# Optimization experiments

Hardware: AMD Instinct MI355X
Metric: run time of the kernel (lower is better)

## Reference

```python
import jax, jax.numpy as jnp
import numpy as np

N_NODES = 1_000_000
N_EDGES = 32_000_000
DC = 16
HIDDEN = 32
EPS = 1e-8
LN_EPS = 1e-5


def _harmonic_encoding(x, dC):
    # x: [n] curvature in [-1,1]; returns [n, dC] (dC even here)
    norm = jnp.clip((x + 1.0) / (2.0 + EPS), 0.0, 1.0)
    freqs = jnp.arange(1, dC // 2 + 1, dtype=x.dtype) * jnp.pi  # [dC/2]
    ang = norm[:, None] * freqs[None, :]                        # [n, dC/2]
    # interleave sin/cos exactly like torch.stack(...,dim=2).view(n,dC)
    return jnp.stack([jnp.sin(ang), jnp.cos(ang)], axis=2).reshape(x.shape[0], dC)


def setup_inputs() -> dict:
    key = jax.random.key(0)
    k_orc, k_ei, k_w1, k_w2, k_g = jax.random.split(key, 5)
    node_orc = jax.random.uniform(k_orc, (N_NODES,), dtype=jnp.float32) * 2.0 - 1.0
    edge_index = jax.random.randint(k_ei, (2, N_EDGES), 0, N_NODES, dtype=jnp.int64)
    # MLP params (torch Linear convention: W [out, in])
    W1 = jax.random.normal(k_w1, (HIDDEN, DC), dtype=jnp.float32) * (1.0 / np.sqrt(DC))
    b1 = jnp.zeros((HIDDEN,), dtype=jnp.float32)
    W2 = jax.random.normal(k_w2, (DC, HIDDEN), dtype=jnp.float32) * (1.0 / np.sqrt(HIDDEN))
    b2 = jnp.zeros((DC,), dtype=jnp.float32)
    gamma = jnp.ones((DC,), dtype=jnp.float32)
    beta = jnp.zeros((DC,), dtype=jnp.float32)
    return {"node_orc": node_orc, "edge_index": edge_index,
            "W1": W1, "b1": b1, "W2": W2, "b2": b2,
            "gamma": gamma, "beta": beta}


def _neighbor_mean(node_orc, edge_index):
    src, dst = edge_index[0], edge_index[1]
    n = node_orc.shape[0]
    deg = jnp.zeros((n,), node_orc.dtype).at[src].add(1.0).at[dst].add(1.0)
    s = (jnp.zeros((n,), node_orc.dtype)
         .at[src].add(node_orc[dst])
         .at[dst].add(node_orc[src]))
    return jnp.where(deg > 0, s / jnp.where(deg > 0, deg, 1.0), 0.0)


def reference(node_orc, edge_index, W1, b1, W2, b2, gamma, beta):
    # advanced harmonic encoding: node encoding + neighbor-mean encoding
    nb_mean = _neighbor_mean(node_orc, edge_index)
    Phi_base = jnp.concatenate(
        [_harmonic_encoding(node_orc, DC // 2),
         _harmonic_encoding(nb_mean, DC // 2)], axis=1)      # [n, 16]
    # learnable MLP (dropout in eval = identity) + LayerNorm + residual
    h = jax.nn.relu(jnp.einsum('nd,hd->nh', Phi_base, W1) + b1)
    y = jnp.einsum('nh,dh->nd', h, W2) + b2
    mu = jnp.mean(y, axis=-1, keepdims=True)
    var = jnp.var(y, axis=-1, keepdims=True)
    y = (y - mu) / jnp.sqrt(var + LN_EPS) * gamma + beta
    return y + Phi_base
```

## Files before the change

kernel.cpp:

```cpp
#include <hip/hip_runtime.h>
#include <hip/hip_bf16.h>

constexpr int kNodes = 1000000;
constexpr int kEdges = 32000000;

constexpr int NB = 256;
constexpr int BSHIFT = 12;
constexpr int BNODES = 4096;
constexpr int NBUSED = (kNodes + BNODES - 1) / BNODES;
constexpr int EPT = 4096;
constexpr int TILES = (kEdges + EPT - 1) / EPT;
constexpr int TSTRIDE = 8960;

constexpr size_t kRecBytes = (size_t)TILES * TSTRIDE * 4;
constexpr size_t kTblOff   = kRecBytes;
constexpr size_t kTblBytes = ((size_t)(NB + 1) * TILES * 2 + 15) & ~(size_t)15;
constexpr size_t kAccOff   = kTblOff + kTblBytes;
constexpr size_t kWsNeeded = kAccOff + (size_t)kNodes * 8;

__global__ __launch_bounds__(512) void scatter_sort(
        const int* __restrict__ ei, const float* __restrict__ orc,
        unsigned* __restrict__ rec, unsigned short* __restrict__ tbl) {
    __shared__ alignas(16) int es[EPT];
    __shared__ alignas(16) int ed[EPT];
    __shared__ alignas(16) unsigned reorder[TSTRIDE];
    __shared__ unsigned cnt[NB];
    __shared__ unsigned scanbuf[NB];
    const int tid = threadIdx.x;
    const int t = blockIdx.x;
    const int e0 = t * EPT;
    const int ne = min(EPT, kEdges - e0);

    for (int k = tid; k < NB; k += 512) cnt[k] = 0u;
    for (int k = tid; k < TSTRIDE; k += 512) reorder[k] = 0xFFFFFFFFu;
    __syncthreads();

    for (int k4 = tid * 4; k4 < ne; k4 += 2048) {
        const int4 s4 = *reinterpret_cast<const int4*>(ei + e0 + k4);
        const int4 d4 = *reinterpret_cast<const int4*>(ei + kEdges + e0 + k4);
        *reinterpret_cast<int4*>(es + k4) = s4;
        *reinterpret_cast<int4*>(ed + k4) = d4;
        atomicAdd(&cnt[s4.x >> BSHIFT], 1u);
        atomicAdd(&cnt[s4.y >> BSHIFT], 1u);
        atomicAdd(&cnt[s4.z >> BSHIFT], 1u);
        atomicAdd(&cnt[s4.w >> BSHIFT], 1u);
        atomicAdd(&cnt[d4.x >> BSHIFT], 1u);
        atomicAdd(&cnt[d4.y >> BSHIFT], 1u);
        atomicAdd(&cnt[d4.z >> BSHIFT], 1u);
        atomicAdd(&cnt[d4.w >> BSHIFT], 1u);
    }
    __syncthreads();

    if (tid < NB) scanbuf[tid] = (cnt[tid] + 3u) & ~3u;
    __syncthreads();
    for (int off = 1; off < NB; off <<= 1) {
        unsigned v = 0u;
        if (tid < NB && tid >= off) v = scanbuf[tid - off];
        __syncthreads();
        if (tid < NB) scanbuf[tid] += v;
        __syncthreads();
    }
    if (tid < NB) {
        const unsigned pc = (cnt[tid] + 3u) & ~3u;
        const unsigned st = scanbuf[tid] - pc;
        tbl[(size_t)tid * TILES + t] = (unsigned short)st;
        cnt[tid] = st;
    }
    if (tid == 0) tbl[(size_t)NB * TILES + t] = (unsigned short)scanbuf[NB - 1];
    __syncthreads();

    for (int k4 = tid * 4; k4 < ne; k4 += 2048) {
        #pragma unroll
        for (int j = 0; j < 4; ++j) {
            const int k = k4 + j;
            const int s = es[k], d = ed[k];
            const float os = orc[s], od = orc[d];
            unsigned qs = __float2uint_rn((od + 1.0f) * 524288.0f);
            unsigned qd = __float2uint_rn((os + 1.0f) * 524288.0f);
            qs = qs > 0xFFFFFu ? 0xFFFFFu : qs;
            qd = qd > 0xFFFFFu ? 0xFFFFFu : qd;
            const unsigned rs = atomicAdd(&cnt[s >> BSHIFT], 1u);
            reorder[rs] = ((unsigned)(s & (BNODES - 1)) << 20) | qs;
            const unsigned rd = atomicAdd(&cnt[d >> BSHIFT], 1u);
            reorder[rd] = ((unsigned)(d & (BNODES - 1)) << 20) | qd;
        }
    }
    __syncthreads();

    const unsigned total = scanbuf[NB - 1];
    unsigned* __restrict__ g = rec + (size_t)t * TSTRIDE;
    for (unsigned k = tid * 4; k < total; k += 2048)
        *reinterpret_cast<int4*>(g + k) = *reinterpret_cast<const int4*>(reorder + k);
}

__global__ __launch_bounds__(512) void bucket_accum(
        const unsigned* __restrict__ rec, const unsigned short* __restrict__ tbl,
        unsigned long long* __restrict__ acc) {
    __shared__ unsigned long long lacc[BNODES];
    const int b = blockIdx.x;
    const int tid = threadIdx.x;
    for (int k = tid; k < BNODES; k += 512) lacc[k] = 0ull;
    __syncthreads();
    const unsigned short* __restrict__ r0 = tbl + (size_t)b * TILES;
    const unsigned short* __restrict__ r1 = tbl + (size_t)(b + 1) * TILES;
    for (int t = tid; t < TILES; t += 512) {
        const unsigned st = r0[t];
        const unsigned en = r1[t];
        const uint4* __restrict__ p =
            reinterpret_cast<const uint4*>(rec + (size_t)t * TSTRIDE + st);
        const unsigned n4 = (en - st) >> 2;
        for (unsigned i = 0; i < n4; ++i) {
            const uint4 v = p[i];
            const unsigned long long a0 = (v.x == 0xFFFFFFFFu) ? 0ull
                : ((1ull << 42) | (unsigned long long)(v.x & 0xFFFFFu));
            atomicAdd(&lacc[v.x >> 20], a0);
            const unsigned long long a1 = (v.y == 0xFFFFFFFFu) ? 0ull
                : ((1ull << 42) | (unsigned long long)(v.y & 0xFFFFFu));
            atomicAdd(&lacc[v.y >> 20], a1);
            const unsigned long long a2 = (v.z == 0xFFFFFFFFu) ? 0ull
                : ((1ull << 42) | (unsigned long long)(v.z & 0xFFFFFu));
            atomicAdd(&lacc[v.z >> 20], a2);
            const unsigned long long a3 = (v.w == 0xFFFFFFFFu) ? 0ull
                : ((1ull << 42) | (unsigned long long)(v.w & 0xFFFFFu));
            atomicAdd(&lacc[v.w >> 20], a3);
        }
    }
    __syncthreads();
    const int base = b << BSHIFT;
    for (int k = tid; k < BNODES; k += 512) {
        const int n = base + k;
        if (n < kNodes) acc[n] = lacc[k];
    }
}

constexpr float kScale = 1048576.0f;
constexpr float kInvScale = 1.0f / 1048576.0f;
constexpr long long kBias = 1ll << 36;

__global__ __launch_bounds__(256) void zero_acc(unsigned long long* __restrict__ acc) {
    int i = blockIdx.x * 256 + threadIdx.x;
    if (i < kNodes) acc[i] = 0ull;
}

__global__ __launch_bounds__(256) void edge_kernel(
        const int* __restrict__ ei,
        const float* __restrict__ orc,
        unsigned long long* __restrict__ acc) {
    int t = blockIdx.x * 256 + threadIdx.x;
    int e0 = t * 4;
    if (e0 >= kEdges) return;
    const int4 s4 = *reinterpret_cast<const int4*>(ei + e0);
    const int4 d4 = *reinterpret_cast<const int4*>(ei + kEdges + e0);
    const int ss[4] = {s4.x, s4.y, s4.z, s4.w};
    const int dd[4] = {d4.x, d4.y, d4.z, d4.w};
    #pragma unroll
    for (int k = 0; k < 4; ++k) {
        const float os = orc[ss[k]];
        const float od = orc[dd[k]];
        const unsigned long long ps =
            (1ull << 48) + (unsigned long long)(kBias + (long long)__float2ll_rn(od * kScale));
        const unsigned long long pd =
            (1ull << 48) + (unsigned long long)(kBias + (long long)__float2ll_rn(os * kScale));
        atomicAdd(&acc[ss[k]], ps);
        atomicAdd(&acc[dd[k]], pd);
    }
}

template <int MODE>
__global__ __launch_bounds__(256) void node_kernel(
        const float* __restrict__ orc,
        const unsigned long long* __restrict__ acc,
        const float* __restrict__ W1, const float* __restrict__ b1,
        const float* __restrict__ W2, const float* __restrict__ b2,
        const float* __restrict__ gamma, const float* __restrict__ beta,
        float* __restrict__ out) {
    const int i = blockIdx.x * 256 + threadIdx.x;
    if (i >= kNodes) return;

    const float x0 = orc[i];
    const unsigned long long p = acc[i];
    float nb;
    if (MODE == 0) {
        const unsigned deg = (unsigned)(p >> 48);
        const long long sf = (long long)(p & ((1ull << 48) - 1)) - (long long)deg * kBias;
        const float s = (float)sf * kInvScale;
        nb = (deg > 0) ? s / (float)deg : 0.0f;
    } else {
        const unsigned deg = (unsigned)(p >> 42);
        const unsigned long long sumq = p & ((1ull << 42) - 1);
        nb = (deg > 0) ? ((float)sumq * (1.0f / 524288.0f) / (float)deg - 1.0f) : 0.0f;
    }

    constexpr float kPi = 3.14159265358979323846f;
    float Phi[16];
    const float n0 = __saturatef((x0 + 1.0f) * 0.5f);
    const float n1 = __saturatef((nb + 1.0f) * 0.5f);
    #pragma unroll
    for (int k = 0; k < 4; ++k) {
        const float a0 = n0 * (float)(k + 1) * kPi;
        const float a1 = n1 * (float)(k + 1) * kPi;
        Phi[2 * k]     = __sinf(a0);
        Phi[2 * k + 1] = __cosf(a0);
        Phi[8 + 2 * k]     = __sinf(a1);
        Phi[8 + 2 * k + 1] = __cosf(a1);
    }

    float y[16];
    #pragma unroll
    for (int d = 0; d < 16; ++d) y[d] = b2[d];
    #pragma unroll
    for (int j = 0; j < 32; ++j) {
        float a = b1[j];
        #pragma unroll
        for (int d = 0; d < 16; ++d) a = fmaf(Phi[d], W1[j * 16 + d], a);
        a = fmaxf(a, 0.0f);
        #pragma unroll
        for (int d = 0; d < 16; ++d) y[d] = fmaf(a, W2[d * 32 + j], y[d]);
    }

    float mu = 0.0f;
    #pragma unroll
    for (int d = 0; d < 16; ++d) mu += y[d];
    mu *= (1.0f / 16.0f);
    float var = 0.0f;
    #pragma unroll
    for (int d = 0; d < 16; ++d) { const float t = y[d] - mu; var = fmaf(t, t, var); }
    var *= (1.0f / 16.0f);
    const float inv = rsqrtf(var + 1e-5f);

    float4* o4 = reinterpret_cast<float4*>(out + (size_t)i * 16);
    #pragma unroll
    for (int q = 0; q < 4; ++q) {
        float4 o;
        o.x = (y[4 * q + 0] - mu) * inv * gamma[4 * q + 0] + beta[4 * q + 0] + Phi[4 * q + 0];
        o.y = (y[4 * q + 1] - mu) * inv * gamma[4 * q + 1] + beta[4 * q + 1] + Phi[4 * q + 1];
        o.z = (y[4 * q + 2] - mu) * inv * gamma[4 * q + 2] + beta[4 * q + 2] + Phi[4 * q + 2];
        o.w = (y[4 * q + 3] - mu) * inv * gamma[4 * q + 3] + beta[4 * q + 3] + Phi[4 * q + 3];
        o4[q] = o;
    }
}

extern "C" void kernel_launch(void* const* d_in, const int* in_sizes, int n_in,
                              void* d_out, int out_size, void* d_ws, size_t ws_size,
                              hipStream_t stream) {
    const float* orc   = (const float*)d_in[0];
    const int*   ei    = (const int*)d_in[1];
    const float* W1    = (const float*)d_in[2];
    const float* b1    = (const float*)d_in[3];
    const float* W2    = (const float*)d_in[4];
    const float* b2    = (const float*)d_in[5];
    const float* gamma = (const float*)d_in[6];
    const float* beta  = (const float*)d_in[7];
    float* out = (float*)d_out;
    char* ws = (char*)d_ws;

    if (ws_size >= kWsNeeded) {
        unsigned* rec = (unsigned*)ws;
        unsigned short* tbl = (unsigned short*)(ws + kTblOff);
        unsigned long long* acc = (unsigned long long*)(ws + kAccOff);
        scatter_sort<<<TILES, 512, 0, stream>>>(ei, orc, rec, tbl);
        bucket_accum<<<NBUSED, 512, 0, stream>>>(rec, tbl, acc);
        node_kernel<2><<<(kNodes + 255) / 256, 256, 0, stream>>>(
            orc, acc, W1, b1, W2, b2, gamma, beta, out);
    } else {
        unsigned long long* acc = (unsigned long long*)ws;
        zero_acc<<<(kNodes + 255) / 256, 256, 0, stream>>>(acc);
        edge_kernel<<<(kEdges / 4 + 255) / 256, 256, 0, stream>>>(ei, orc, acc);
        node_kernel<0><<<(kNodes + 255) / 256, 256, 0, stream>>>(
            orc, acc, W1, b1, W2, b2, gamma, beta, out);
    }
}
```

Measured before the change: 866.8 us.

## Quantize node values to 16 bits and use 32-bit split-bucket LDS accumulation

A new prepass quantizes node curvature to 16-bit codes so the edge gathers read half the bytes. Edge records shrink to a 12-bit local node index plus a 16-bit value. The bucket accumulator switches from 64-bit to 32-bit LDS atomics, packing an 8-bit degree with a 24-bit sum, and each bucket is split across two blocks whose partial sums are combined in the node kernel. The scatter kernel now uses 1024 threads with one int4 per thread and no staging arrays in shared memory, and replaces the block-wide prefix scan with a wave shuffle scan. Padding records go to a dummy LDS slot, which removes a per-record branch. The cost is coarser quantization of the neighbor mean, an extra small kernel, and a limit on per-half degree and sum range.

Result: faster. 724.0 us (-16.5%).

```diff
diff --git a/kernel.cpp b/kernel.cpp
--- a/kernel.cpp
+++ b/kernel.cpp
@@ -1,5 +1,4 @@
 #include <hip/hip_runtime.h>
-#include <hip/hip_bf16.h>
 
 constexpr int kNodes = 1000000;
 constexpr int kEdges = 32000000;
@@ -11,99 +10,149 @@
 constexpr int EPT = 4096;
 constexpr int TILES = (kEdges + EPT - 1) / EPT;
 constexpr int TSTRIDE = 8960;
-
-constexpr size_t kRecBytes = (size_t)TILES * TSTRIDE * 4;
-constexpr size_t kTblOff   = kRecBytes;
-constexpr size_t kTblBytes = ((size_t)(NB + 1) * TILES * 2 + 15) & ~(size_t)15;
-constexpr size_t kAccOff   = kTblOff + kTblBytes;
-constexpr size_t kWsNeeded = kAccOff + (size_t)kNodes * 8;
-
-__global__ __launch_bounds__(512) void scatter_sort(
-        const int* __restrict__ ei, const float* __restrict__ orc,
+constexpr unsigned PADREC = 0x10000000u;
+constexpr int SPLIT = 2;
+
+constexpr size_t kRecBytes  = (size_t)TILES * TSTRIDE * 4;
+constexpr size_t kTblOff    = kRecBytes;
+constexpr size_t kTblBytes  = ((size_t)(NB + 1) * TILES * 2 + 15) & ~(size_t)15;
+constexpr size_t kAccOff    = kTblOff + kTblBytes;
+constexpr size_t kAccBytes  = (size_t)SPLIT * kNodes * 4;
+constexpr size_t kOrcqOff   = kAccOff + kAccBytes;
+constexpr size_t kOrcqBytes = (size_t)kNodes * 2;
+constexpr size_t kWsNeeded  = kOrcqOff + kOrcqBytes;
+
+__global__ __launch_bounds__(256) void quant_orc(
+        const float* __restrict__ orc, unsigned short* __restrict__ orcq) {
+    const int i = (blockIdx.x * 256 + threadIdx.x) * 4;
+    if (i >= kNodes) return;
+    const float4 v = *reinterpret_cast<const float4*>(orc + i);
+    unsigned q0 = __float2uint_rn((v.x + 1.0f) * 32768.0f);
+    unsigned q1 = __float2uint_rn((v.y + 1.0f) * 32768.0f);
+    unsigned q2 = __float2uint_rn((v.z + 1.0f) * 32768.0f);
+    unsigned q3 = __float2uint_rn((v.w + 1.0f) * 32768.0f);
+    q0 = q0 > 65535u ? 65535u : q0;
+    q1 = q1 > 65535u ? 65535u : q1;
+    q2 = q2 > 65535u ? 65535u : q2;
+    q3 = q3 > 65535u ? 65535u : q3;
+    ushort4 q;
+    q.x = (unsigned short)q0; q.y = (unsigned short)q1;
+    q.z = (unsigned short)q2; q.w = (unsigned short)q3;
+    *reinterpret_cast<ushort4*>(orcq + i) = q;
+}
+
+__global__ __launch_bounds__(1024) void scatter_sort(
+        const int* __restrict__ ei, const unsigned short* __restrict__ orcq,
         unsigned* __restrict__ rec, unsigned short* __restrict__ tbl) {
-    __shared__ alignas(16) int es[EPT];
-    __shared__ alignas(16) int ed[EPT];
     __shared__ alignas(16) unsigned reorder[TSTRIDE];
     __shared__ unsigned cnt[NB];
-    __shared__ unsigned scanbuf[NB];
+    __shared__ unsigned totsh;
     const int tid = threadIdx.x;
     const int t = blockIdx.x;
     const int e0 = t * EPT;
     const int ne = min(EPT, kEdges - e0);
-
-    for (int k = tid; k < NB; k += 512) cnt[k] = 0u;
-    for (int k = tid; k < TSTRIDE; k += 512) reorder[k] = 0xFFFFFFFFu;
-    __syncthreads();
-
-    for (int k4 = tid * 4; k4 < ne; k4 += 2048) {
-        const int4 s4 = *reinterpret_cast<const int4*>(ei + e0 + k4);
-        const int4 d4 = *reinterpret_cast<const int4*>(ei + kEdges + e0 + k4);
-        *reinterpret_cast<int4*>(es + k4) = s4;
-        *reinterpret_cast<int4*>(ed + k4) = d4;
-        atomicAdd(&cnt[s4.x >> BSHIFT], 1u);
-        atomicAdd(&cnt[s4.y >> BSHIFT], 1u);
-        atomicAdd(&cnt[s4.z >> BSHIFT], 1u);
-        atomicAdd(&cnt[s4.w >> BSHIFT], 1u);
-        atomicAdd(&cnt[d4.x >> BSHIFT], 1u);
-        atomicAdd(&cnt[d4.y >> BSHIFT], 1u);
-        atomicAdd(&cnt[d4.z >> BSHIFT], 1u);
-        atomicAdd(&cnt[d4.w >> BSHIFT], 1u);
-    }
-    __syncthreads();
-
-    if (tid < NB) scanbuf[tid] = (cnt[tid] + 3u) & ~3u;
-    __syncthreads();
-    for (int off = 1; off < NB; off <<= 1) {
-        unsigned v = 0u;
-        if (tid < NB && tid >= off) v = scanbuf[tid - off];
-        __syncthreads();
-        if (tid < NB) scanbuf[tid] += v;
-        __syncthreads();
-    }
-    if (tid < NB) {
-        const unsigned pc = (cnt[tid] + 3u) & ~3u;
-        const unsigned st = scanbuf[tid] - pc;
-        tbl[(size_t)tid * TILES + t] = (unsigned short)st;
-        cnt[tid] = st;
-    }
-    if (tid == 0) tbl[(size_t)NB * TILES + t] = (unsigned short)scanbuf[NB - 1];
-    __syncthreads();
-
-    for (int k4 = tid * 4; k4 < ne; k4 += 2048) {
+    const int k4 = tid * 4;
+
+    {
+        int4 p4; p4.x = p4.y = p4.z = p4.w = (int)PADREC;
+        for (int k = k4; k < TSTRIDE; k += 4096)
+            *reinterpret_cast<int4*>(reorder + k) = p4;
+    }
+    if (tid < NB) cnt[tid] = 0u;
+    __syncthreads();
+
+    int4 s4, d4;
+    s4.x = s4.y = s4.z = s4.w = 0; d4 = s4;
+    unsigned pq0 = 0, pq1 = 0, pq2 = 0, pq3 = 0;
+    const bool act = k4 < ne;
+    if (act) {
+        s4 = *reinterpret_cast<const int4*>(ei + e0 + k4);
+        d4 = *reinterpret_cast<const int4*>(ei + kEdges + e0 + k4);
+        const unsigned a0 = orcq[d4.x], a1 = orcq[d4.y],
+                       a2 = orcq[d4.z], a3 = orcq[d4.w];
+        const unsigned b0 = orcq[s4.x], b1 = orcq[s4.y],
+                       b2 = orcq[s4.z], b3 = orcq[s4.w];
+        atomicAdd(&cnt[(unsigned)s4.x >> BSHIFT], 1u);
+        atomicAdd(&cnt[(unsigned)s4.y >> BSHIFT], 1u);
+        atomicAdd(&cnt[(unsigned)s4.z >> BSHIFT], 1u);
+        atomicAdd(&cnt[(unsigned)s4.w >> BSHIFT], 1u);
+        atomicAdd(&cnt[(unsigned)d4.x >> BSHIFT], 1u);
+        atomicAdd(&cnt[(unsigned)d4.y >> BSHIFT], 1u);
+        atomicAdd(&cnt[(unsigned)d4.z >> BSHIFT], 1u);
+        atomicAdd(&cnt[(unsigned)d4.w >> BSHIFT], 1u);
+        pq0 = a0 | (b0 << 16);
+        pq1 = a1 | (b1 << 16);
+        pq2 = a2 | (b2 << 16);
+        pq3 = a3 | (b3 << 16);
+    }
+    __syncthreads();
+
+    if (tid < 64) {
+        unsigned c0 = cnt[4 * tid + 0], c1 = cnt[4 * tid + 1];
+        unsigned c2 = cnt[4 * tid + 2], c3 = cnt[4 * tid + 3];
+        c0 = (c0 + 3u) & ~3u; c1 = (c1 + 3u) & ~3u;
+        c2 = (c2 + 3u) & ~3u; c3 = (c3 + 3u) & ~3u;
+        const unsigned loc = c0 + c1 + c2 + c3;
+        unsigned inc = loc;
         #pragma unroll
-        for (int j = 0; j < 4; ++j) {
-            const int k = k4 + j;
-            const int s = es[k], d = ed[k];
-            const float os = orc[s], od = orc[d];
-            unsigned qs = __float2uint_rn((od + 1.0f) * 524288.0f);
-            unsigned qd = __float2uint_rn((os + 1.0f) * 524288.0f);
-            qs = qs > 0xFFFFFu ? 0xFFFFFu : qs;
-            qd = qd > 0xFFFFFu ? 0xFFFFFu : qd;
-            const unsigned rs = atomicAdd(&cnt[s >> BSHIFT], 1u);
-            reorder[rs] = ((unsigned)(s & (BNODES - 1)) << 20) | qs;
-            const unsigned rd = atomicAdd(&cnt[d >> BSHIFT], 1u);
-            reorder[rd] = ((unsigned)(d & (BNODES - 1)) << 20) | qd;
+        for (int d = 1; d < 64; d <<= 1) {
+            const unsigned v = (unsigned)__shfl_up((int)inc, d, 64);
+            if (tid >= d) inc += v;
         }
-    }
-    __syncthreads();
-
-    const unsigned total = scanbuf[NB - 1];
+        unsigned base = inc - loc;
+        cnt[4 * tid + 0] = base;
+        tbl[(size_t)(4 * tid + 0) * TILES + t] = (unsigned short)base;
+        base += c0;
+        cnt[4 * tid + 1] = base;
+        tbl[(size_t)(4 * tid + 1) * TILES + t] = (unsigned short)base;
+        base += c1;
+        cnt[4 * tid + 2] = base;
+        tbl[(size_t)(4 * tid + 2) * TILES + t] = (unsigned short)base;
+        base += c2;
+        cnt[4 * tid + 3] = base;
+        tbl[(size_t)(4 * tid + 3) * TILES + t] = (unsigned short)base;
+        if (tid == 63) {
+            totsh = inc;
+            tbl[(size_t)NB * TILES + t] = (unsigned short)inc;
+        }
+    }
+    __syncthreads();
+
+    if (act) {
+        #define RANK1(S, D, PQ) { \
+            const unsigned rs_ = atomicAdd(&cnt[(unsigned)(S) >> BSHIFT], 1u); \
+            reorder[rs_] = (((unsigned)(S) & (BNODES - 1)) << 16) | ((PQ) & 0xFFFFu); \
+            const unsigned rd_ = atomicAdd(&cnt[(unsigned)(D) >> BSHIFT], 1u); \
+            reorder[rd_] = (((unsigned)(D) & (BNODES - 1)) << 16) | ((PQ) >> 16); }
+        RANK1(s4.x, d4.x, pq0)
+        RANK1(s4.y, d4.y, pq1)
+        RANK1(s4.z, d4.z, pq2)
+        RANK1(s4.w, d4.w, pq3)
+        #undef RANK1
+    }
+    __syncthreads();
+
+    const unsigned total = totsh;
     unsigned* __restrict__ g = rec + (size_t)t * TSTRIDE;
-    for (unsigned k = tid * 4; k < total; k += 2048)
+    for (unsigned k = (unsigned)k4; k < total; k += 4096)
         *reinterpret_cast<int4*>(g + k) = *reinterpret_cast<const int4*>(reorder + k);
 }
 
-__global__ __launch_bounds__(512) void bucket_accum(
+__global__ __launch_bounds__(1024) void bucket_accum(
         const unsigned* __restrict__ rec, const unsigned short* __restrict__ tbl,
-        unsigned long long* __restrict__ acc) {
-    __shared__ unsigned long long lacc[BNODES];
-    const int b = blockIdx.x;
+        unsigned* __restrict__ acc) {
+    __shared__ unsigned lacc[BNODES + 4];
     const int tid = threadIdx.x;
-    for (int k = tid; k < BNODES; k += 512) lacc[k] = 0ull;
-    __syncthreads();
+    const int b = blockIdx.x >> 1;
+    const int half = blockIdx.x & 1;
+    for (int k = tid; k < BNODES + 4; k += 1024) lacc[k] = 0u;
+    __syncthreads();
+    constexpr int TPS = (TILES + SPLIT - 1) / SPLIT;
+    const int t0 = half * TPS;
+    const int t1 = min(TILES, t0 + TPS);
     const unsigned short* __restrict__ r0 = tbl + (size_t)b * TILES;
     const unsigned short* __restrict__ r1 = tbl + (size_t)(b + 1) * TILES;
-    for (int t = tid; t < TILES; t += 512) {
+    for (int t = t0 + tid; t < t1; t += 1024) {
         const unsigned st = r0[t];
         const unsigned en = r1[t];
         const uint4* __restrict__ p =
@@ -111,25 +160,18 @@
         const unsigned n4 = (en - st) >> 2;
         for (unsigned i = 0; i < n4; ++i) {
             const uint4 v = p[i];
-            const unsigned long long a0 = (v.x == 0xFFFFFFFFu) ? 0ull
-                : ((1ull << 42) | (unsigned long long)(v.x & 0xFFFFFu));
-            atomicAdd(&lacc[v.x >> 20], a0);
-            const unsigned long long a1 = (v.y == 0xFFFFFFFFu) ? 0ull
-                : ((1ull << 42) | (unsigned long long)(v.y & 0xFFFFFu));
-            atomicAdd(&lacc[v.y >> 20], a1);
-            const unsigned long long a2 = (v.z == 0xFFFFFFFFu) ? 0ull
-                : ((1ull << 42) | (unsigned long long)(v.z & 0xFFFFFu));
-            atomicAdd(&lacc[v.z >> 20], a2);
-            const unsigned long long a3 = (v.w == 0xFFFFFFFFu) ? 0ull
-                : ((1ull << 42) | (unsigned long long)(v.w & 0xFFFFFu));
-            atomicAdd(&lacc[v.w >> 20], a3);
+            atomicAdd(&lacc[v.x >> 16], (v.x & 0xFFFFu) | 0x1000000u);
+            atomicAdd(&lacc[v.y >> 16], (v.y & 0xFFFFu) | 0x1000000u);
+            atomicAdd(&lacc[v.z >> 16], (v.z & 0xFFFFu) | 0x1000000u);
+            atomicAdd(&lacc[v.w >> 16], (v.w & 0xFFFFu) | 0x1000000u);
         }
     }
     __syncthreads();
     const int base = b << BSHIFT;
-    for (int k = tid; k < BNODES; k += 512) {
+    unsigned* __restrict__ dst = acc + (size_t)half * kNodes;
+    for (int k = tid; k < BNODES; k += 1024) {
         const int n = base + k;
-        if (n < kNodes) acc[n] = lacc[k];
+        if (n < kNodes) dst[n] = lacc[k];
     }
 }
 
@@ -169,7 +211,8 @@
 template <int MODE>
 __global__ __launch_bounds__(256) void node_kernel(
         const float* __restrict__ orc,
-        const unsigned long long* __restrict__ acc,
+        const unsigned long long* __restrict__ acc64,
+        const unsigned* __restrict__ acc32,
         const float* __restrict__ W1, const float* __restrict__ b1,
         const float* __restrict__ W2, const float* __restrict__ b2,
         const float* __restrict__ gamma, const float* __restrict__ beta,
@@ -178,17 +221,20 @@
     if (i >= kNodes) return;
 
     const float x0 = orc[i];
-    const unsigned long long p = acc[i];
     float nb;
     if (MODE == 0) {
+        const unsigned long long p = acc64[i];
         const unsigned deg = (unsigned)(p >> 48);
         const long long sf = (long long)(p & ((1ull << 48) - 1)) - (long long)deg * kBias;
         const float s = (float)sf * kInvScale;
         nb = (deg > 0) ? s / (float)deg : 0.0f;
     } else {
-        const unsigned deg = (unsigned)(p >> 42);
-        const unsigned long long sumq = p & ((1ull << 42) - 1);
-        nb = (deg > 0) ? ((float)sumq * (1.0f / 524288.0f) / (float)deg - 1.0f) : 0.0f;
+        const unsigned p0 = acc32[i];
+        const unsigned p1 = acc32[kNodes + i];
+        const unsigned deg = (p0 >> 24) + (p1 >> 24);
+        const unsigned sumq = (p0 & 0xFFFFFFu) + (p1 & 0xFFFFFFu);
+        nb = (deg > 0)
+            ? ((float)sumq * (1.0f / 32768.0f) / (float)deg - 1.0f) : 0.0f;
     }
 
     constexpr float kPi = 3.14159265358979323846f;
@@ -257,16 +303,18 @@
     if (ws_size >= kWsNeeded) {
         unsigned* rec = (unsigned*)ws;
         unsigned short* tbl = (unsigned short*)(ws + kTblOff);
-        unsigned long long* acc = (unsigned long long*)(ws + kAccOff);
-        scatter_sort<<<TILES, 512, 0, stream>>>(ei, orc, rec, tbl);
-        bucket_accum<<<NBUSED, 512, 0, stream>>>(rec, tbl, acc);
-        node_kernel<2><<<(kNodes + 255) / 256, 256, 0, stream>>>(
-            orc, acc, W1, b1, W2, b2, gamma, beta, out);
+        unsigned* acc = (unsigned*)(ws + kAccOff);
+        unsigned short* orcq = (unsigned short*)(ws + kOrcqOff);
+        quant_orc<<<(kNodes / 4 + 255) / 256, 256, 0, stream>>>(orc, orcq);
+        scatter_sort<<<TILES, 1024, 0, stream>>>(ei, orcq, rec, tbl);
+        bucket_accum<<<NBUSED * SPLIT, 1024, 0, stream>>>(rec, tbl, acc);
+        node_kernel<3><<<(kNodes + 255) / 256, 256, 0, stream>>>(
+            orc, nullptr, acc, W1, b1, W2, b2, gamma, beta, out);
     } else {
         unsigned long long* acc = (unsigned long long*)ws;
         zero_acc<<<(kNodes + 255) / 256, 256, 0, stream>>>(acc);
         edge_kernel<<<(kEdges / 4 + 255) / 256, 256, 0, stream>>>(ei, orc, acc);
         node_kernel<0><<<(kNodes + 255) / 256, 256, 0, stream>>>(
-            orc, acc, W1, b1, W2, b2, gamma, beta, out);
-    }
-}
+            orc, acc, nullptr, W1, b1, W2, b2, gamma, beta, out);
+    }
+}
```
